# Optimization experiments

Hardware: AMD Instinct MI355X
Metric: run time of the kernel (lower is better)

## Reference

```python
import jax, jax.numpy as jnp
import numpy as np


def setup_inputs() -> dict:
    key = jax.random.key(0)
    k1, k2 = jax.random.split(key)
    N, D_IN, D_OUT, R = 500000, 128, 128, 8
    inputs = jax.random.normal(k1, (N, D_IN), dtype=jnp.float32)
    # glorot-uniform-ish init for relation weights
    limit = np.sqrt(6.0 / (D_IN + D_OUT)).astype(np.float32)
    relation_weights = jax.random.uniform(k2, (R, D_IN, D_OUT), dtype=jnp.float32, minval=-limit, maxval=limit)
    relation_scales = jnp.ones((R, 1), dtype=jnp.float32)
    return {"inputs": inputs, "relation_weights": relation_weights, "relation_scales": relation_scales}


def reference(inputs, relation_weights, relation_scales):
    # Original: sum_i  inputs @ (W_i * s_i)
    # Algebraically identical: inputs @ sum_i (W_i * s_i) -> one GEMM.
    # scales: [R,1] -> broadcast over [R, d_in, d_out]
    W_eff = jnp.sum(relation_weights * relation_scales[:, :, None], axis=0)  # [d_in, d_out]
    return inputs @ W_eff  # [N, d_out]
```

## Files before the change

kernel.cpp:

```cpp
#include <hip/hip_runtime.h>

typedef __attribute__((ext_vector_type(8))) short short8;
typedef __attribute__((ext_vector_type(4))) float f32x4;

__device__ __forceinline__ short f2bf(float f) {
    unsigned u = __builtin_bit_cast(unsigned, f);
    u += 0x7fffu + ((u >> 16) & 1u);
    return (short)(u >> 16);
}

__global__ void weff_kernel(const float* __restrict__ W,
                            const float* __restrict__ S,
                            short* __restrict__ WT) {
    int idx = blockIdx.x * 256 + threadIdx.x;
    int k = idx >> 7;
    int n = idx & 127;
    float acc = 0.f;
#pragma unroll
    for (int r = 0; r < 8; ++r) acc += S[r] * W[r * 16384 + idx];
    WT[n * 128 + k] = f2bf(acc);
}

#define BSTRIDE 136

__global__ __launch_bounds__(256, 3) void gemm_kernel(const float* __restrict__ A,
                                                      const short* __restrict__ WT,
                                                      float* __restrict__ C,
                                                      int N, int nchunks) {
    __shared__ __align__(16) short Bs[128 * BSTRIDE];

    int tid = threadIdx.x;
#pragma unroll
    for (int it = 0; it < 8; ++it) {
        int chunk = it * 256 + tid;
        int n  = chunk >> 4;
        int kc = chunk & 15;
        *(short8*)&Bs[n * BSTRIDE + kc * 8] = ((const short8*)WT)[chunk];
    }
    __syncthreads();

    int wave = tid >> 6;
    int lane = tid & 63;
    int quad = lane >> 4;
    int r16  = lane & 15;

    const short* bbase = &Bs[r16 * BSTRIDE];
    int stride = gridDim.x;

    f32x4 cur[8], nxt[8];

    int c0 = blockIdx.x;
    {
        int rowA = c0 * 64 + wave * 16 + r16;
        if (rowA >= N) rowA = N - 1;
        const float* arow = A + (long)rowA * 128;
#pragma unroll
        for (int kk = 0; kk < 4; ++kk) {
            cur[kk * 2]     = *(const f32x4*)(arow + kk * 32 + quad * 8);
            cur[kk * 2 + 1] = *(const f32x4*)(arow + kk * 32 + quad * 8 + 4);
        }
    }

    for (int c = c0; c < nchunks; c += stride) {
        int cn = c + stride;
        if (cn < nchunks) {
            int rowA = cn * 64 + wave * 16 + r16;
            if (rowA >= N) rowA = N - 1;
            const float* arow = A + (long)rowA * 128;
#pragma unroll
            for (int kk = 0; kk < 4; ++kk) {
                nxt[kk * 2]     = *(const f32x4*)(arow + kk * 32 + quad * 8);
                nxt[kk * 2 + 1] = *(const f32x4*)(arow + kk * 32 + quad * 8 + 4);
            }
        }

        f32x4 acc[8];
#pragma unroll
        for (int t = 0; t < 8; ++t) acc[t] = (f32x4)(0.f);

#pragma unroll
        for (int kk = 0; kk < 4; ++kk) {
            f32x4 p = cur[kk * 2];
            f32x4 q = cur[kk * 2 + 1];
            short8 afrag;
            afrag[0] = f2bf(p[0]); afrag[1] = f2bf(p[1]);
            afrag[2] = f2bf(p[2]); afrag[3] = f2bf(p[3]);
            afrag[4] = f2bf(q[0]); afrag[5] = f2bf(q[1]);
            afrag[6] = f2bf(q[2]); afrag[7] = f2bf(q[3]);
            const short* bk = bbase + kk * 32 + quad * 8;
#pragma unroll
            for (int t = 0; t < 8; ++t) {
                short8 bfrag = *(const short8*)(bk + t * 16 * BSTRIDE);
                acc[t] = __builtin_amdgcn_mfma_f32_16x16x32_bf16(bfrag, afrag, acc[t], 0, 0, 0);
            }
        }

        int row = c * 64 + wave * 16 + r16;
        if (row < N) {
            float* crow = C + (long)row * 128 + quad * 4;
#pragma unroll
            for (int t = 0; t < 8; ++t) {
                __builtin_nontemporal_store(acc[t], (f32x4*)(crow + t * 16));
            }
        }

#pragma unroll
        for (int i = 0; i < 8; ++i) cur[i] = nxt[i];
    }
}

extern "C" void kernel_launch(void* const* d_in, const int* in_sizes, int n_in,
                              void* d_out, int out_size, void* d_ws, size_t ws_size,
                              hipStream_t stream) {
    const float* inputs = (const float*)d_in[0];
    const float* W      = (const float*)d_in[1];
    const float* S      = (const float*)d_in[2];
    float* out = (float*)d_out;
    short* WT  = (short*)d_ws;

    int N = in_sizes[0] / 128;

    weff_kernel<<<64, 256, 0, stream>>>(W, S, WT);

    int nchunks = (N + 63) / 64;
    int grid = nchunks < 1024 ? nchunks : 1024;
    gemm_kernel<<<grid, 256, 0, stream>>>(inputs, WT, out, N, nchunks);
}
```

Before: 483.1 us.

## Use 512-thread blocks with per-wave 16-row work items in GEMM

Moves the GEMM kernel from 256-thread blocks that process 64-row chunks to 512-thread blocks whose eight waves each independently grid-stride over 16-row items. The launch uses up to 768 blocks and a launch bound of 6 blocks per CU. This amortizes the per-block shared-memory load of the weight matrix over twice as many waves and balances work at wave granularity. The higher occupancy target may constrain registers and cause spills, and per-wave striding changes the memory access locality across the block.

```diff
diff --git a/kernel.cpp b/kernel.cpp
--- a/kernel.cpp
+++ b/kernel.cpp
@@ -23,16 +23,16 @@
 
 #define BSTRIDE 136
 
-__global__ __launch_bounds__(256, 3) void gemm_kernel(const float* __restrict__ A,
+__global__ __launch_bounds__(512, 6) void gemm_kernel(const float* __restrict__ A,
                                                       const short* __restrict__ WT,
                                                       float* __restrict__ C,
-                                                      int N, int nchunks) {
+                                                      int N, int nitems) {
     __shared__ __align__(16) short Bs[128 * BSTRIDE];
 
     int tid = threadIdx.x;
 #pragma unroll
-    for (int it = 0; it < 8; ++it) {
-        int chunk = it * 256 + tid;
+    for (int itv = 0; itv < 4; ++itv) {
+        int chunk = itv * 512 + tid;
         int n  = chunk >> 4;
         int kc = chunk & 15;
         *(short8*)&Bs[n * BSTRIDE + kc * 8] = ((const short8*)WT)[chunk];
@@ -45,15 +45,16 @@
     int r16  = lane & 15;
 
     const short* bbase = &Bs[r16 * BSTRIDE];
-    int stride = gridDim.x;
+
+    int gw = blockIdx.x * 8 + wave;
+    int nw = gridDim.x * 8;
 
     f32x4 cur[8], nxt[8];
 
-    int c0 = blockIdx.x;
     {
-        int rowA = c0 * 64 + wave * 16 + r16;
+        long rowA = (long)gw * 16 + r16;
         if (rowA >= N) rowA = N - 1;
-        const float* arow = A + (long)rowA * 128;
+        const float* arow = A + rowA * 128;
 #pragma unroll
         for (int kk = 0; kk < 4; ++kk) {
             cur[kk * 2]     = *(const f32x4*)(arow + kk * 32 + quad * 8);
@@ -61,12 +62,12 @@
         }
     }
 
-    for (int c = c0; c < nchunks; c += stride) {
-        int cn = c + stride;
-        if (cn < nchunks) {
-            int rowA = cn * 64 + wave * 16 + r16;
+    for (int it = gw; it < nitems; it += nw) {
+        int itn = it + nw;
+        if (itn < nitems) {
+            long rowA = (long)itn * 16 + r16;
             if (rowA >= N) rowA = N - 1;
-            const float* arow = A + (long)rowA * 128;
+            const float* arow = A + rowA * 128;
 #pragma unroll
             for (int kk = 0; kk < 4; ++kk) {
                 nxt[kk * 2]     = *(const f32x4*)(arow + kk * 32 + quad * 8);
@@ -95,9 +96,9 @@
             }
         }
 
-        int row = c * 64 + wave * 16 + r16;
+        long row = (long)it * 16 + r16;
         if (row < N) {
-            float* crow = C + (long)row * 128 + quad * 4;
+            float* crow = C + row * 128 + quad * 4;
 #pragma unroll
             for (int t = 0; t < 8; ++t) {
                 __builtin_nontemporal_store(acc[t], (f32x4*)(crow + t * 16));
@@ -122,7 +123,9 @@
 
     weff_kernel<<<64, 256, 0, stream>>>(W, S, WT);
 
-    int nchunks = (N + 63) / 64;
-    int grid = nchunks < 1024 ? nchunks : 1024;
-    gemm_kernel<<<grid, 256, 0, stream>>>(inputs, WT, out, N, nchunks);
+    int nitems = (N + 15) / 16;
+    int grid = 768;
+    int maxg = (nitems + 7) / 8;
+    if (grid > maxg) grid = maxg;
+    gemm_kernel<<<grid, 512, 0, stream>>>(inputs, WT, out, N, nitems);
 }
```

Result: slower. 686.8 us (+42.2%).
